# Optimization experiments

Hardware: AMD Instinct MI355X
Metric: run time of the kernel (lower is better)

Reference implementation:

```python
import jax, jax.numpy as jnp
import numpy as np

D_MODEL = 512
N_HEADS = 8
D_K = D_MODEL // N_HEADS
WINDOW = 32  # attention restricted to |i-j| <= WINDOW//2
SCALE = float(np.sqrt(D_K))


def setup_inputs() -> dict:
    key = jax.random.key(0)
    ks = jax.random.split(key, 11)
    B, S, D = 2, 4096, D_MODEL
    inv = 1.0 / np.sqrt(D)
    inp = {
        "query": jax.random.normal(ks[0], (B, S, D), jnp.float32),
        "key": jax.random.normal(ks[1], (B, S, D), jnp.float32),
        "value": jax.random.normal(ks[2], (B, S, D), jnp.float32),
        # torch nn.Linear params: weight (out,in), bias (out,)
        "wq": jax.random.uniform(ks[3], (D, D), jnp.float32, -inv, inv),
        "bq": jax.random.uniform(ks[4], (D,), jnp.float32, -inv, inv),
        "wk": jax.random.uniform(ks[5], (D, D), jnp.float32, -inv, inv),
        "bk": jax.random.uniform(ks[6], (D,), jnp.float32, -inv, inv),
        "wv": jax.random.uniform(ks[7], (D, D), jnp.float32, -inv, inv),
        "bv": jax.random.uniform(ks[8], (D,), jnp.float32, -inv, inv),
        "wo": jax.random.uniform(ks[9], (D, D), jnp.float32, -inv, inv),
        "bo": jax.random.uniform(ks[10], (D,), jnp.float32, -inv, inv),
    }
    return inp


def _linear(x, w, b):
    # torch: y = x @ w.T + b
    return jnp.einsum('bsd,od->bso', x, w) + b


def reference(query, key, value, wq, bq, wk, bk, wv, bv, wo, bo):
    B, S, D = query.shape
    # project and split heads -> [B, H, S, d_k]
    def split(x):
        return x.reshape(B, S, N_HEADS, D_K).transpose(0, 2, 1, 3)
    Q = split(_linear(query, wq, bq))
    K = split(_linear(key, wk, bk))
    V = split(_linear(value, wv, bv))
    # full scores then banded mask (faithful to original dense-masked impl)
    scores = jnp.einsum('bhqd,bhkd->bhqk', Q, K) / SCALE
    i = jnp.arange(S)[:, None]
    j = jnp.arange(S)[None, :]
    band = jnp.abs(i - j) <= (WINDOW // 2)  # [S, S]
    scores = jnp.where(band[None, None, :, :], scores, -1e9)
    attn = jax.nn.softmax(scores, axis=-1)
    ctx = jnp.einsum('bhqk,bhkd->bhqd', attn, V)
    ctx = ctx.transpose(0, 2, 1, 3).reshape(B, S, D)
    return _linear(ctx, wo, bo)
```

## Files before the change

kernel.cpp:

```cpp
#include <hip/hip_runtime.h>
#include <hip/hip_bf16.h>

using u16 = unsigned short;
using u32 = unsigned int;

typedef float f32x4 __attribute__((ext_vector_type(4)));
typedef __bf16 bf16x8 __attribute__((ext_vector_type(8)));

constexpr int B_ = 2;
constexpr int S_ = 4096;
constexpr int D_ = 512;
constexpr int H_ = 8;
constexpr int DK_ = 64;
constexpr int M_ = B_ * S_;
constexpr int K_ = 512;

__device__ __forceinline__ float bf2f(u16 u) {
  return __uint_as_float(((u32)u) << 16);
}
__device__ __forceinline__ u16 f2bf(float x) {
  u32 u = __float_as_uint(x);
  u = (u + 0x7fffu + ((u >> 16) & 1u)) >> 16;
  return (u16)u;
}
__device__ __forceinline__ u32 pack2(float a, float b) {
  return (u32)f2bf(a) | ((u32)f2bf(b) << 16);
}

__device__ __forceinline__ void gload16(const u16* g, u16* l) {
  __builtin_amdgcn_global_load_lds((const __attribute__((address_space(1))) void*)g,
                                   (__attribute__((address_space(3))) void*)l,
                                   16, 0, 0);
}

constexpr int NG_ACT = 3 * (4194304 / 8);
constexpr int NG_W   = 4 * (262144 / 8);
constexpr int NG_ALL = NG_ACT + NG_W;

__global__ __launch_bounds__(256) void convert_all(
    const float* __restrict__ q, const float* __restrict__ k, const float* __restrict__ v,
    const float* __restrict__ wq, const float* __restrict__ wk,
    const float* __restrict__ wv, const float* __restrict__ wo,
    u16* __restrict__ qb, u16* __restrict__ kb, u16* __restrict__ vb,
    u16* __restrict__ wqb, u16* __restrict__ wkb, u16* __restrict__ wvb,
    u16* __restrict__ wob)
{
  const int g8 = blockIdx.x * 256 + threadIdx.x;
  if (g8 >= NG_ALL) return;
  const float* s; u16* d; size_t off;
  if (g8 < NG_ACT) {
    const int t = g8 / (4194304 / 8);
    const int r = g8 - t * (4194304 / 8);
    s = (t == 0) ? q : (t == 1) ? k : v;
    d = (t == 0) ? qb : (t == 1) ? kb : vb;
    off = (size_t)r * 8;
  } else {
    const int g2 = g8 - NG_ACT;
    const int t = g2 >> 15;
    const int r = g2 & 32767;
    s = (t == 0) ? wq : (t == 1) ? wk : (t == 2) ? wv : wo;
    d = (t == 0) ? wqb : (t == 1) ? wkb : (t == 2) ? wvb : wob;
    off = (size_t)r * 8;
  }
  const float4 x = *(const float4*)(s + off);
  const float4 y = *(const float4*)(s + off + 4);
  uint4 o;
  o.x = pack2(x.x, x.y); o.y = pack2(x.z, x.w);
  o.z = pack2(y.x, y.y); o.w = pack2(y.z, y.w);
  *(uint4*)(d + off) = o;
}

template<int MODE>
__device__ __forceinline__ void gemm_body(const u16* __restrict__ A,
                                          const u16* __restrict__ Wt,
                                          const float* __restrict__ bias,
                                          void* __restrict__ Cout,
                                          u16* __restrict__ As,
                                          u16* __restrict__ Bs)
{
  const int tid  = threadIdx.x;
  const int lane = tid & 63;
  const int w    = tid >> 6;
  const int wm   = w >> 1;
  const int wn   = w & 1;
  const int m0   = blockIdx.x * 128;
  const int n0   = blockIdx.y * 128;
  const int qr   = lane & 15;
  const int g    = lane >> 4;

  const int swz8 = (((lane & 7) ^ (lane >> 3))) * 8;
  const u16* a0 = A  + (size_t)(m0 + w * 32 + (lane >> 3)) * K_ + swz8;
  const u16* b0 = Wt + (size_t)(n0 + w * 32 + (lane >> 3)) * K_ + swz8;

  auto stage = [&](int t) {
#pragma unroll
    for (int p = 0; p < 4; ++p)
      gload16(a0 + t * 64 + (size_t)p * 8 * K_, &As[(w * 32 + p * 8) * 64]);
#pragma unroll
    for (int p = 0; p < 4; ++p)
      gload16(b0 + t * 64 + (size_t)p * 8 * K_, &Bs[(w * 32 + p * 8) * 64]);
  };

  f32x4 acc[4][4] = {};

  stage(0);

  const int ax = (qr & 7) << 4;
  const char* ab = (const char*)As + (wm * 64 + qr) * 128;
  const char* bb = (const char*)Bs + (wn * 64 + qr) * 128;

  constexpr int NT = K_ / 64;
#pragma unroll 1
  for (int t = 0; t < NT; ++t) {
    __syncthreads();

#pragma unroll
    for (int kk = 0; kk < 2; ++kk) {
      bf16x8 af[4], bfr[4];
#pragma unroll
      for (int i = 0; i < 4; ++i)
        af[i]  = *(const bf16x8*)(ab + i * 2048 + ((g * 16 + kk * 64) ^ ax));
#pragma unroll
      for (int j = 0; j < 4; ++j)
        bfr[j] = *(const bf16x8*)(bb + j * 2048 + ((g * 16 + kk * 64) ^ ax));
#pragma unroll
      for (int i = 0; i < 4; ++i)
#pragma unroll
        for (int j = 0; j < 4; ++j)
          acc[i][j] = __builtin_amdgcn_mfma_f32_16x16x32_bf16(af[i], bfr[j], acc[i][j], 0, 0, 0);
    }

    if (t + 1 < NT) {
      __syncthreads();
      stage(t + 1);
    }
  }

#pragma unroll
  for (int j = 0; j < 4; ++j) {
    const int col = n0 + wn * 64 + j * 16 + qr;
    const float bv = bias[col];
#pragma unroll
    for (int i = 0; i < 4; ++i) {
      const int rbase = m0 + wm * 64 + i * 16 + g * 4;
      if constexpr (MODE == 2) {
        const int bb2 = rbase >> 12;
        const int ss = rbase & (S_ - 1);
        const int hh = col >> 6;
        const int dd = col & (DK_ - 1);
        uint2 pk;
        pk.x = pack2(acc[i][j][0] + bv, acc[i][j][1] + bv);
        pk.y = pack2(acc[i][j][2] + bv, acc[i][j][3] + bv);
        *(uint2*)&((u16*)Cout)[((size_t)((bb2 * H_ + hh) * DK_ + dd)) * S_ + ss] = pk;
      } else {
#pragma unroll
        for (int r = 0; r < 4; ++r) {
          const int row = rbase + r;
          const float vv = acc[i][j][r] + bv;
          if constexpr (MODE == 0) {
            ((float*)Cout)[(size_t)row * D_ + col] = vv;
          } else {
            const int bb2 = row >> 12;
            const int ss = row & (S_ - 1);
            const int hh = col >> 6;
            const int dd = col & (DK_ - 1);
            ((u16*)Cout)[((size_t)(bb2 * H_ + hh) * S_ + ss) * DK_ + dd] = f2bf(vv);
          }
        }
      }
    }
  }
}

__global__ __launch_bounds__(256, 4) void gemm_qkv(
    const u16* __restrict__ qb, const u16* __restrict__ kb, const u16* __restrict__ vb,
    const u16* __restrict__ wqb, const u16* __restrict__ wkb, const u16* __restrict__ wvb,
    const float* __restrict__ bq, const float* __restrict__ bk, const float* __restrict__ bv,
    u16* __restrict__ Qo, u16* __restrict__ Ko, u16* __restrict__ Vo)
{
  __shared__ u16 As[128 * 64];
  __shared__ u16 Bs[128 * 64];
  if (blockIdx.z == 0)      gemm_body<1>(qb, wqb, bq, Qo, As, Bs);
  else if (blockIdx.z == 1) gemm_body<1>(kb, wkb, bk, Ko, As, Bs);
  else                      gemm_body<2>(vb, wvb, bv, Vo, As, Bs);
}

__global__ __launch_bounds__(256, 4) void gemm_out(
    const u16* __restrict__ A, const u16* __restrict__ Wb,
    const float* __restrict__ bias, float* __restrict__ C)
{
  __shared__ u16 As[128 * 64];
  __shared__ u16 Bs[128 * 64];
  gemm_body<0>(A, Wb, bias, C, As, Bs);
}

__global__ __launch_bounds__(256) void attn_band_mfma(
    const u16* __restrict__ Q, const u16* __restrict__ K,
    const u16* __restrict__ Vt, u16* __restrict__ Ctx)
{
  constexpr int LDP = 72;
  __shared__ u16 P_lds[4][16 * LDP];

  const int lane = threadIdx.x & 63;
  const int w    = threadIdx.x >> 6;
  const int wid  = blockIdx.x * 4 + w;
  const int q0   = (wid & 255) << 4;
  const int bh   = wid >> 8;
  const size_t kbase = (size_t)bh * S_ * DK_;

  u16* pl = &P_lds[w][0];
  const int qr = lane & 15;
  const int g  = lane >> 4;

  *(uint2*)&pl[qr * LDP + 48 + 4 * g] = make_uint2(0u, 0u);

  bf16x8 qf[2];
  {
    const u16* qp = Q + kbase + (size_t)(q0 + qr) * DK_ + 8 * g;
    qf[0] = *(const bf16x8*)qp;
    qf[1] = *(const bf16x8*)(qp + 32);
  }

  f32x4 sc[3];
#pragma unroll
  for (int t = 0; t < 3; ++t) {
    int j = q0 - 16 + 16 * t + qr;
    j = min(max(j, 0), S_ - 1);
    const u16* kp = K + kbase + (size_t)j * DK_ + 8 * g;
    const bf16x8 kf0 = *(const bf16x8*)kp;
    const bf16x8 kf1 = *(const bf16x8*)(kp + 32);
    f32x4 a = {};
    a = __builtin_amdgcn_mfma_f32_16x16x32_bf16(kf0, qf[0], a, 0, 0, 0);
    a = __builtin_amdgcn_mfma_f32_16x16x32_bf16(kf1, qf[1], a, 0, 0, 0);
    sc[t] = a;
  }

  float s[3][4];
  float mx = -INFINITY;
#pragma unroll
  for (int t = 0; t < 3; ++t)
#pragma unroll
    for (int r = 0; r < 4; ++r) {
      const int joff = 16 * t + 4 * g + r;
      const int j = q0 - 16 + joff;
      const bool ok = (joff >= qr) && (joff <= qr + 32) && (j >= 0) && (j < S_);
      const float v = ok ? sc[t][r] * 0.125f : -INFINITY;
      s[t][r] = v;
      mx = fmaxf(mx, v);
    }
  mx = fmaxf(mx, __shfl_xor(mx, 16));
  mx = fmaxf(mx, __shfl_xor(mx, 32));

  float p[3][4];
  float den = 0.f;
#pragma unroll
  for (int t = 0; t < 3; ++t)
#pragma unroll
    for (int r = 0; r < 4; ++r) {
      p[t][r] = __expf(s[t][r] - mx);
      den += p[t][r];
    }
  den += __shfl_xor(den, 16);
  den += __shfl_xor(den, 32);
  const float inv = 1.0f / den;

#pragma unroll
  for (int t = 0; t < 3; ++t) {
    uint2 pk;
    pk.x = pack2(p[t][0] * inv, p[t][1] * inv);
    pk.y = pack2(p[t][2] * inv, p[t][3] * inv);
    *(uint2*)&pl[qr * LDP + 16 * t + 4 * g] = pk;
  }

  f32x4 cacc[4] = {};
#pragma unroll
  for (int jc = 0; jc < 2; ++jc) {
    const bf16x8 pa = *(const bf16x8*)&pl[qr * LDP + 8 * g + 32 * jc];
#pragma unroll
    for (int nt = 0; nt < 4; ++nt) {
      int jj = q0 - 16 + 8 * g + 32 * jc;
      jj = min(max(jj, 0), S_ - 8);
      const u16* vp = Vt + ((size_t)bh * DK_ + 16 * nt + qr) * S_ + jj;
      const bf16x8 vf = *(const bf16x8*)vp;
      cacc[nt] = __builtin_amdgcn_mfma_f32_16x16x32_bf16(pa, vf, cacc[nt], 0, 0, 0);
    }
  }

  const int bb = bh >> 3;
  const int hh = bh & (H_ - 1);
#pragma unroll
  for (int nt = 0; nt < 4; ++nt)
#pragma unroll
    for (int r = 0; r < 4; ++r) {
      const int qq = 4 * g + r;
      const int dd = 16 * nt + qr;
      Ctx[((size_t)(bb * S_ + q0 + qq)) * D_ + hh * DK_ + dd] = f2bf(cacc[nt][r]);
    }
}

extern "C" void kernel_launch(void* const* d_in, const int* in_sizes, int n_in,
                              void* d_out, int out_size, void* d_ws, size_t ws_size,
                              hipStream_t stream)
{
  const float* query = (const float*)d_in[0];
  const float* key   = (const float*)d_in[1];
  const float* value = (const float*)d_in[2];
  const float* wq    = (const float*)d_in[3];
  const float* bq    = (const float*)d_in[4];
  const float* wk    = (const float*)d_in[5];
  const float* bk    = (const float*)d_in[6];
  const float* wv    = (const float*)d_in[7];
  const float* bv    = (const float*)d_in[8];
  const float* wo    = (const float*)d_in[9];
  const float* bo    = (const float*)d_in[10];

  const size_t seg = (size_t)M_ * D_;
  u16* Qw  = (u16*)d_ws;
  u16* Kw  = Qw + seg;
  u16* Vw  = Kw + seg;
  u16* qb  = Vw + seg;
  u16* kb  = qb + seg;
  u16* vb  = kb + seg;
  u16* wqb = vb + seg;
  u16* wkb = wqb + (size_t)D_ * D_;
  u16* wvb = wkb + (size_t)D_ * D_;
  u16* wob = wvb + (size_t)D_ * D_;
  u16* Cw  = qb;

  dim3 blk(256);
  convert_all<<<dim3((NG_ALL + 255) / 256), blk, 0, stream>>>(
      query, key, value, wq, wk, wv, wo, qb, kb, vb, wqb, wkb, wvb, wob);
  gemm_qkv<<<dim3(M_ / 128, D_ / 128, 3), blk, 0, stream>>>(
      qb, kb, vb, wqb, wkb, wvb, bq, bk, bv, Qw, Kw, Vw);
  attn_band_mfma<<<dim3((B_ * H_ * S_) / 64), blk, 0, stream>>>(Qw, Kw, Vw, Cw);
  gemm_out<<<dim3(M_ / 128, D_ / 128), blk, 0, stream>>>(Cw, wob, bo, (float*)d_out);
}
```

Before: 60.75 us.

## Fuse fp32-to-bf16 activation conversion into QKV GEMM A-tile loading

The separate conversion pass over the query, key and value activations is removed. The QKV GEMM now reads fp32 A tiles straight from global memory into registers, packs them to bf16 and writes them into a swizzled LDS tile, with half of the next tile's loads issued before the MFMA loop. Only the weights are still converted up front. This drops a full write and re-read of the bf16 activation copies. In exchange the GEMM loads twice the bytes per A tile and uses register-staged loads instead of direct-to-LDS loads, which may hide latency less well. gemm_out keeps its original bf16 direct-load path, inlined as its own kernel.

New measurement: 68.54 us. +12.8%, slower.

```diff
diff --git a/kernel.cpp b/kernel.cpp
--- a/kernel.cpp
+++ b/kernel.cpp
@@ -33,35 +33,21 @@
                                    16, 0, 0);
 }
 
-constexpr int NG_ACT = 3 * (4194304 / 8);
-constexpr int NG_W   = 4 * (262144 / 8);
-constexpr int NG_ALL = NG_ACT + NG_W;
-
-__global__ __launch_bounds__(256) void convert_all(
-    const float* __restrict__ q, const float* __restrict__ k, const float* __restrict__ v,
+constexpr int NG_W = 4 * (262144 / 8);
+
+__global__ __launch_bounds__(256) void convert_w(
     const float* __restrict__ wq, const float* __restrict__ wk,
     const float* __restrict__ wv, const float* __restrict__ wo,
-    u16* __restrict__ qb, u16* __restrict__ kb, u16* __restrict__ vb,
     u16* __restrict__ wqb, u16* __restrict__ wkb, u16* __restrict__ wvb,
     u16* __restrict__ wob)
 {
   const int g8 = blockIdx.x * 256 + threadIdx.x;
-  if (g8 >= NG_ALL) return;
-  const float* s; u16* d; size_t off;
-  if (g8 < NG_ACT) {
-    const int t = g8 / (4194304 / 8);
-    const int r = g8 - t * (4194304 / 8);
-    s = (t == 0) ? q : (t == 1) ? k : v;
-    d = (t == 0) ? qb : (t == 1) ? kb : vb;
-    off = (size_t)r * 8;
-  } else {
-    const int g2 = g8 - NG_ACT;
-    const int t = g2 >> 15;
-    const int r = g2 & 32767;
-    s = (t == 0) ? wq : (t == 1) ? wk : (t == 2) ? wv : wo;
-    d = (t == 0) ? wqb : (t == 1) ? wkb : (t == 2) ? wvb : wob;
-    off = (size_t)r * 8;
-  }
+  if (g8 >= NG_W) return;
+  const int t = g8 >> 15;
+  const int r = g8 & 32767;
+  const float* s = (t == 0) ? wq : (t == 1) ? wk : (t == 2) ? wv : wo;
+  u16* d = (t == 0) ? wqb : (t == 1) ? wkb : (t == 2) ? wvb : wob;
+  const size_t off = (size_t)r * 8;
   const float4 x = *(const float4*)(s + off);
   const float4 y = *(const float4*)(s + off + 4);
   uint4 o;
@@ -71,12 +57,12 @@
 }
 
 template<int MODE>
-__device__ __forceinline__ void gemm_body(const u16* __restrict__ A,
-                                          const u16* __restrict__ Wt,
-                                          const float* __restrict__ bias,
-                                          void* __restrict__ Cout,
-                                          u16* __restrict__ As,
-                                          u16* __restrict__ Bs)
+__device__ __forceinline__ void gemm_body_f32A(const float* __restrict__ A,
+                                               const u16* __restrict__ Wt,
+                                               const float* __restrict__ bias,
+                                               void* __restrict__ Cout,
+                                               u16* __restrict__ As,
+                                               u16* __restrict__ Bs)
 {
   const int tid  = threadIdx.x;
   const int lane = tid & 63;
@@ -88,14 +74,26 @@
   const int qr   = lane & 15;
   const int g    = lane >> 4;
 
-  const int swz8 = (((lane & 7) ^ (lane >> 3))) * 8;
-  const u16* a0 = A  + (size_t)(m0 + w * 32 + (lane >> 3)) * K_ + swz8;
+  const int sr8 = tid >> 3;
+  const int c8  = tid & 7;
+  const float* afp = A + (size_t)(m0 + sr8) * K_ + c8 * 8;
+  char* awr = (char*)As + sr8 * 128 + ((c8 ^ (sr8 & 7)) * 16);
+
+  auto a_load = [&](int t, int p, float4& x, float4& y) {
+    const float* s = afp + t * 64 + (size_t)p * 32 * K_;
+    x = *(const float4*)s;
+    y = *(const float4*)(s + 4);
+  };
+  auto a_write = [&](int p, const float4& x, const float4& y) {
+    uint4 o;
+    o.x = pack2(x.x, x.y); o.y = pack2(x.z, x.w);
+    o.z = pack2(y.x, y.y); o.w = pack2(y.z, y.w);
+    *(uint4*)(awr + p * 32 * 128) = o;
+  };
+
+  const int swz8 = ((lane & 7) ^ (lane >> 3)) * 8;
   const u16* b0 = Wt + (size_t)(n0 + w * 32 + (lane >> 3)) * K_ + swz8;
-
-  auto stage = [&](int t) {
-#pragma unroll
-    for (int p = 0; p < 4; ++p)
-      gload16(a0 + t * 64 + (size_t)p * 8 * K_, &As[(w * 32 + p * 8) * 64]);
+  auto stage_B = [&](int t) {
 #pragma unroll
     for (int p = 0; p < 4; ++p)
       gload16(b0 + t * 64 + (size_t)p * 8 * K_, &Bs[(w * 32 + p * 8) * 64]);
@@ -103,7 +101,14 @@
 
   f32x4 acc[4][4] = {};
 
-  stage(0);
+  {
+    float4 x0, y0, x1, y1, x2, y2, x3, y3;
+    a_load(0, 0, x0, y0); a_load(0, 1, x1, y1);
+    a_load(0, 2, x2, y2); a_load(0, 3, x3, y3);
+    a_write(0, x0, y0); a_write(1, x1, y1);
+    a_write(2, x2, y2); a_write(3, x3, y3);
+    stage_B(0);
+  }
 
   const int ax = (qr & 7) << 4;
   const char* ab = (const char*)As + (wm * 64 + qr) * 128;
@@ -114,6 +119,12 @@
   for (int t = 0; t < NT; ++t) {
     __syncthreads();
 
+    float4 xa, ya, xb, yb;
+    if (t + 1 < NT) {
+      a_load(t + 1, 0, xa, ya);
+      a_load(t + 1, 1, xb, yb);
+    }
+
 #pragma unroll
     for (int kk = 0; kk < 2; ++kk) {
       bf16x8 af[4], bfr[4];
@@ -132,7 +143,11 @@
 
     if (t + 1 < NT) {
       __syncthreads();
-      stage(t + 1);
+      a_write(0, xa, ya); a_write(1, xb, yb);
+      float4 xc, yc, xd, yd;
+      a_load(t + 1, 2, xc, yc); a_load(t + 1, 3, xd, yd);
+      a_write(2, xc, yc); a_write(3, xd, yd);
+      stage_B(t + 1);
     }
   }
 
@@ -156,16 +171,12 @@
 #pragma unroll
         for (int r = 0; r < 4; ++r) {
           const int row = rbase + r;
-          const float vv = acc[i][j][r] + bv;
-          if constexpr (MODE == 0) {
-            ((float*)Cout)[(size_t)row * D_ + col] = vv;
-          } else {
-            const int bb2 = row >> 12;
-            const int ss = row & (S_ - 1);
-            const int hh = col >> 6;
-            const int dd = col & (DK_ - 1);
-            ((u16*)Cout)[((size_t)(bb2 * H_ + hh) * S_ + ss) * DK_ + dd] = f2bf(vv);
-          }
+          const int bb2 = row >> 12;
+          const int ss = row & (S_ - 1);
+          const int hh = col >> 6;
+          const int dd = col & (DK_ - 1);
+          ((u16*)Cout)[((size_t)(bb2 * H_ + hh) * S_ + ss) * DK_ + dd] =
+              f2bf(acc[i][j][r] + bv);
         }
       }
     }
@@ -173,25 +184,92 @@
 }
 
 __global__ __launch_bounds__(256, 4) void gemm_qkv(
-    const u16* __restrict__ qb, const u16* __restrict__ kb, const u16* __restrict__ vb,
+    const float* __restrict__ q, const float* __restrict__ k, const float* __restrict__ v,
     const u16* __restrict__ wqb, const u16* __restrict__ wkb, const u16* __restrict__ wvb,
     const float* __restrict__ bq, const float* __restrict__ bk, const float* __restrict__ bv,
     u16* __restrict__ Qo, u16* __restrict__ Ko, u16* __restrict__ Vo)
 {
   __shared__ u16 As[128 * 64];
   __shared__ u16 Bs[128 * 64];
-  if (blockIdx.z == 0)      gemm_body<1>(qb, wqb, bq, Qo, As, Bs);
-  else if (blockIdx.z == 1) gemm_body<1>(kb, wkb, bk, Ko, As, Bs);
-  else                      gemm_body<2>(vb, wvb, bv, Vo, As, Bs);
+  if (blockIdx.z == 0)      gemm_body_f32A<1>(q, wqb, bq, Qo, As, Bs);
+  else if (blockIdx.z == 1) gemm_body_f32A<1>(k, wkb, bk, Ko, As, Bs);
+  else                      gemm_body_f32A<2>(v, wvb, bv, Vo, As, Bs);
 }
 
 __global__ __launch_bounds__(256, 4) void gemm_out(
-    const u16* __restrict__ A, const u16* __restrict__ Wb,
+    const u16* __restrict__ A, const u16* __restrict__ Wt,
     const float* __restrict__ bias, float* __restrict__ C)
 {
   __shared__ u16 As[128 * 64];
   __shared__ u16 Bs[128 * 64];
-  gemm_body<0>(A, Wb, bias, C, As, Bs);
+
+  const int tid  = threadIdx.x;
+  const int lane = tid & 63;
+  const int w    = tid >> 6;
+  const int wm   = w >> 1;
+  const int wn   = w & 1;
+  const int m0   = blockIdx.x * 128;
+  const int n0   = blockIdx.y * 128;
+  const int qr   = lane & 15;
+  const int g    = lane >> 4;
+
+  const int swz8 = ((lane & 7) ^ (lane >> 3)) * 8;
+  const u16* a0 = A  + (size_t)(m0 + w * 32 + (lane >> 3)) * K_ + swz8;
+  const u16* b0 = Wt + (size_t)(n0 + w * 32 + (lane >> 3)) * K_ + swz8;
+
+  auto stage = [&](int t) {
+#pragma unroll
+    for (int p = 0; p < 4; ++p)
+      gload16(a0 + t * 64 + (size_t)p * 8 * K_, &As[(w * 32 + p * 8) * 64]);
+#pragma unroll
+    for (int p = 0; p < 4; ++p)
+      gload16(b0 + t * 64 + (size_t)p * 8 * K_, &Bs[(w * 32 + p * 8) * 64]);
+  };
+
+  f32x4 acc[4][4] = {};
+  stage(0);
+
+  const int ax = (qr & 7) << 4;
+  const char* ab = (const char*)As + (wm * 64 + qr) * 128;
+  const char* bb = (const char*)Bs + (wn * 64 + qr) * 128;
+
+  constexpr int NT = K_ / 64;
+#pragma unroll 1
+  for (int t = 0; t < NT; ++t) {
+    __syncthreads();
+#pragma unroll
+    for (int kk = 0; kk < 2; ++kk) {
+      bf16x8 af[4], bfr[4];
+#pragma unroll
+      for (int i = 0; i < 4; ++i)
+        af[i]  = *(const bf16x8*)(ab + i * 2048 + ((g * 16 + kk * 64) ^ ax));
+#pragma unroll
+      for (int j = 0; j < 4; ++j)
+        bfr[j] = *(const bf16x8*)(bb + j * 2048 + ((g * 16 + kk * 64) ^ ax));
+#pragma unroll
+      for (int i = 0; i < 4; ++i)
+#pragma unroll
+        for (int j = 0; j < 4; ++j)
+          acc[i][j] = __builtin_amdgcn_mfma_f32_16x16x32_bf16(af[i], bfr[j], acc[i][j], 0, 0, 0);
+    }
+    if (t + 1 < NT) {
+      __syncthreads();
+      stage(t + 1);
+    }
+  }
+
+#pragma unroll
+  for (int j = 0; j < 4; ++j) {
+    const int col = n0 + wn * 64 + j * 16 + qr;
+    const float bv = bias[col];
+#pragma unroll
+    for (int i = 0; i < 4; ++i) {
+      const int rbase = m0 + wm * 64 + i * 16 + g * 4;
+#pragma unroll
+      for (int r = 0; r < 4; ++r)
+        C[(size_t)(rbase + r) * D_ + col] = acc[i][j][r] + bv;
+    }
+  }
 }
 
 __global__ __launch_bounds__(256) void attn_band_mfma(
@@ -318,20 +396,17 @@
   u16* Qw  = (u16*)d_ws;
   u16* Kw  = Qw + seg;
   u16* Vw  = Kw + seg;
-  u16* qb  = Vw + seg;
-  u16* kb  = qb + seg;
-  u16* vb  = kb + seg;
-  u16* wqb = vb + seg;
+  u16* Cw  = Vw + seg;
+  u16* wqb = Cw + seg;
   u16* wkb = wqb + (size_t)D_ * D_;
   u16* wvb = wkb + (size_t)D_ * D_;
   u16* wob = wvb + (size_t)D_ * D_;
-  u16* Cw  = qb;
 
   dim3 blk(256);
-  convert_all<<<dim3((NG_ALL + 255) / 256), blk, 0, stream>>>(
-      query, key, value, wq, wk, wv, wo, qb, kb, vb, wqb, wkb, wvb, wob);
+  convert_w<<<dim3((NG_W + 255) / 256), blk, 0, stream>>>(
+      wq, wk, wv, wo, wqb, wkb, wvb, wob);
   gemm_qkv<<<dim3(M_ / 128, D_ / 128, 3), blk, 0, stream>>>(
-      qb, kb, vb, wqb, wkb, wvb, bq, bk, bv, Qw, Kw, Vw);
+      query, key, value, wqb, wkb, wvb, bq, bk, bv, Qw, Kw, Vw);
   attn_band_mfma<<<dim3((B_ * H_ * S_) / 64), blk, 0, stream>>>(Qw, Kw, Vw, Cw);
   gemm_out<<<dim3(M_ / 128, D_ / 128), blk, 0, stream>>>(Cw, wob, bo, (float*)d_out);
 }
```
